# Performance work log

Measured on AMD Instinct MI355X. Metric: run time of the kernel, lower is better.

Reference implementation:

```python
import jax, jax.numpy as jnp
import numpy as np

B, N, M = 4, 2048, 2048
DIM, DIM_KEYS, DIM_OUT = 512, 512, 512
HEADS, DIM_HEAD = 8, 64
INNER = HEADS * DIM_HEAD


def setup_inputs() -> dict:
    key = jax.random.key(0)
    ks = jax.random.split(key, 8)
    x = jax.random.normal(ks[0], (B, N, DIM), dtype=jnp.float32)
    context = jax.random.normal(ks[1], (B, M, DIM_KEYS), dtype=jnp.float32)
    Wq = jax.random.normal(ks[2], (DIM, INNER), dtype=jnp.float32) / np.sqrt(DIM)
    Wkv = jax.random.normal(ks[3], (DIM_KEYS, 2 * INNER), dtype=jnp.float32) / np.sqrt(DIM_KEYS)
    null_k = jax.random.normal(ks[4], (DIM_HEAD,), dtype=jnp.float32)
    null_v = jax.random.normal(ks[5], (DIM_HEAD,), dtype=jnp.float32)
    Wout = jax.random.normal(ks[6], (INNER, DIM_OUT), dtype=jnp.float32) / np.sqrt(INNER)
    bout = jnp.zeros((DIM_OUT,), dtype=jnp.float32)
    return {"x": x, "context": context, "Wq": Wq, "Wkv": Wkv,
            "null_k": null_k, "null_v": null_v, "Wout": Wout, "bout": bout}


def reference(x, context, Wq, Wkv, null_k, null_v, Wout, bout):
    b = x.shape[0]
    scale = DIM_HEAD ** (-0.5)
    q = x @ Wq                      # [b, n, inner]
    kv = context @ Wkv              # [b, m, 2*inner]
    k, v = jnp.split(kv, 2, axis=-1)
    # [b, h, n, d]
    q = q.reshape(b, -1, HEADS, DIM_HEAD).transpose(0, 2, 1, 3)
    k = k.reshape(b, -1, HEADS, DIM_HEAD).transpose(0, 2, 1, 3)
    v = v.reshape(b, -1, HEADS, DIM_HEAD).transpose(0, 2, 1, 3)
    # prepend null key/value token: [b, h, 1, d]
    nk = jnp.broadcast_to(null_k, (b, HEADS, 1, DIM_HEAD))
    nv = jnp.broadcast_to(null_v, (b, HEADS, 1, DIM_HEAD))
    k = jnp.concatenate((nk, k), axis=-2)  # [b, h, m+1, d]
    v = jnp.concatenate((nv, v), axis=-2)
    q = jnp.tanh(q)
    k = jnp.tanh(k)
    sim = jnp.einsum('bhid,bhjd->bhij', q, k) * scale  # [b, h, n, m+1]
    attn = jax.nn.softmax(sim, axis=-1)
    out = jnp.einsum('bhij,bhjd->bhid', attn, v)       # [b, h, n, d]
    out = out.transpose(0, 2, 1, 3).reshape(b, -1, INNER)  # [b, n, inner]
    return out @ Wout + bout
```

## Files before the change

kernel.cpp:

```cpp
#include <hip/hip_runtime.h>
#include <hip/hip_bf16.h>
#include <stdint.h>

#define B_    4
#define N_    2048
#define M_    2048
#define DIMX  512
#define INNER 512
#define H_    8
#define DH    64
#define MK    2049
#define MKP   2112

#define QSCALE  0.18033688011f
#define SM_BIAS -11.5415605f

using u16 = unsigned short;
using u32 = unsigned int;

typedef __attribute__((ext_vector_type(8))) short short8;
typedef __attribute__((ext_vector_type(4))) float f32x4;

#if defined(__has_builtin)
# if __has_builtin(__builtin_amdgcn_exp2f)
#  define EXP2(x) __builtin_amdgcn_exp2f(x)
# endif
#endif
#ifndef EXP2
# define EXP2(x) exp2f(x)
#endif

__device__ __forceinline__ u16 bfc(float f){
  __hip_bfloat16 h = __float2bfloat16(f);
  return *reinterpret_cast<u16*>(&h);
}
__device__ __forceinline__ u32 bfpk(float lo, float hi){
  return (u32)bfc(lo) | ((u32)bfc(hi) << 16);
}

__global__ __launch_bounds__(256) void convert_bf(
    const float* __restrict__ x, const float* __restrict__ ctx,
    u16* __restrict__ xb, u16* __restrict__ cb)
{
  const float* in = blockIdx.z ? ctx : x;
  u16* out        = blockIdx.z ? cb : xb;
  const int i = blockIdx.x * 256 + threadIdx.x;
  float4 a = ((const float4*)in)[i*2];
  float4 b = ((const float4*)in)[i*2+1];
  uint4 t;
  t.x = bfpk(a.x, a.y); t.y = bfpk(a.z, a.w);
  t.z = bfpk(b.x, b.y); t.w = bfpk(b.z, b.w);
  ((uint4*)out)[i] = t;
}

__global__ __launch_bounds__(256) void transpose_all(
    const float* __restrict__ Wq, const float* __restrict__ Wkv,
    const float* __restrict__ Wout,
    u16* __restrict__ Wqt, u16* __restrict__ Wkvt, u16* __restrict__ Woutt)
{
  const int z = blockIdx.z;
  const float* in = (z == 0) ? Wq : (z == 1) ? Wkv : Wout;
  u16* out        = (z == 0) ? Wqt : (z == 1) ? Wkvt : Woutt;
  const int C     = (z == 1) ? 1024 : 512;
  const int R     = 512;
  if (blockIdx.x * 64 >= C) return;

  __shared__ float tl[64][65];
  const int t = threadIdx.x;
  const int c0 = blockIdx.x * 64, r0 = blockIdx.y * 64;
  const int col = t & 63, rb = t >> 6;
  #pragma unroll
  for (int j = 0; j < 16; ++j){
    const int row = rb + j*4;
    tl[row][col] = in[(size_t)(r0 + row) * C + c0 + col];
  }
  __syncthreads();
  #pragma unroll
  for (int j = 0; j < 16; ++j){
    const int orow = rb + j*4;
    out[(size_t)(c0 + orow) * R + r0 + col] = bfc(tl[col][orow]);
  }
}

#define PROJ_COMPUTE(bi)                                                      \
  {                                                                           \
    short8 af[4], bf[4];                                                      \
    _Pragma("unroll")                                                         \
    for (int m = 0; m < 4; ++m){                                              \
      const int row = wr + m*16 + c;                                          \
      af[m] = *(const short8*)((char*)At[bi] + row*64 + ((g ^ ((row>>1)&3)) << 4)); \
    }                                                                         \
    _Pragma("unroll")                                                         \
    for (int n = 0; n < 4; ++n){                                              \
      const int row = wc + n*16 + c;                                          \
      bf[n] = *(const short8*)((char*)Bl[bi] + row*64 + ((g ^ ((row>>1)&3)) << 4)); \
    }                                                                         \
    __builtin_amdgcn_s_setprio(1);                                            \
    _Pragma("unroll")                                                         \
    for (int m = 0; m < 4; ++m)                                               \
      _Pragma("unroll")                                                       \
      for (int n = 0; n < 4; ++n)                                             \
        acc[m][n] = __builtin_amdgcn_mfma_f32_16x16x32_bf16(af[m], bf[n], acc[m][n], 0, 0, 0); \
    __builtin_amdgcn_s_setprio(0);                                            \
  }

__global__ __launch_bounds__(256, 3) void fused_proj(
    const u16* __restrict__ xb, const u16* __restrict__ cb,
    const u16* __restrict__ Wqt, const u16* __restrict__ Wkvt,
    u16* __restrict__ qb, u16* __restrict__ kb, u16* __restrict__ vb)
{
  __shared__ __align__(16) short At[2][128*32];
  __shared__ __align__(16) short Bl[2][128*32];

  const int flat = blockIdx.x;
  const int tile = (flat & 7) * 96 + (flat >> 3);
  const bool isq = tile < 256;
  const int lt   = isq ? tile : tile - 256;
  const int gx   = isq ? 4 : 8;
  const int row0 = (lt / gx) * 128, col0 = (lt % gx) * 128;
  const u16* A  = isq ? xb : cb;
  const u16* Bt = isq ? Wqt : Wkvt;

  const int tid = threadIdx.x;
  const int w = tid >> 6, lane = tid & 63;
  const int c = lane & 15, g = lane >> 4;
  const int wr = (w >> 1) * 64, wc = (w & 1) * 64;

  f32x4 acc[4][4] = {};

  const int srow = tid >> 1, sj = (tid & 1) * 2;
  const int swz0 = ((sj  ) ^ ((srow >> 1) & 3)) << 4;
  const int swz1 = ((sj+1) ^ ((srow >> 1) & 3)) << 4;

  const u16* asrc = A  + (size_t)(row0 + srow) * DIMX + sj*8;
  const u16* bsrc = Bt + (size_t)(col0 + srow) * DIMX + sj*8;

  uint4 aA0, aA1, bA0, bA1;
  uint4 aB0, aB1, bB0, bB1;

  aA0 = ((const uint4*)asrc)[0];        aA1 = ((const uint4*)asrc)[1];
  bA0 = ((const uint4*)bsrc)[0];        bA1 = ((const uint4*)bsrc)[1];
  aB0 = ((const uint4*)(asrc + 32))[0]; aB1 = ((const uint4*)(asrc + 32))[1];
  bB0 = ((const uint4*)(bsrc + 32))[0]; bB1 = ((const uint4*)(bsrc + 32))[1];
  *(uint4*)((char*)At[0] + srow*64 + swz0) = aA0;
  *(uint4*)((char*)At[0] + srow*64 + swz1) = aA1;
  *(uint4*)((char*)Bl[0] + srow*64 + swz0) = bA0;
  *(uint4*)((char*)Bl[0] + srow*64 + swz1) = bA1;

  for (int kk = 0; kk < 16; kk += 2){
    __syncthreads();
    if (kk + 2 < 16){
      const u16* an = asrc + (kk+2)*32;
      const u16* bn = bsrc + (kk+2)*32;
      aA0 = ((const uint4*)an)[0]; aA1 = ((const uint4*)an)[1];
      bA0 = ((const uint4*)bn)[0]; bA1 = ((const uint4*)bn)[1];
    }
    PROJ_COMPUTE(0);
    *(uint4*)((char*)At[1] + srow*64 + swz0) = aB0;
    *(uint4*)((char*)At[1] + srow*64 + swz1) = aB1;
    *(uint4*)((char*)Bl[1] + srow*64 + swz0) = bB0;
    *(uint4*)((char*)Bl[1] + srow*64 + swz1) = bB1;

    __syncthreads();
    if (kk + 3 < 16){
      const u16* an = asrc + (kk+3)*32;
      const u16* bn = bsrc + (kk+3)*32;
      aB0 = ((const uint4*)an)[0]; aB1 = ((const uint4*)an)[1];
      bB0 = ((const uint4*)bn)[0]; bB1 = ((const uint4*)bn)[1];
    }
    PROJ_COMPUTE(1);
    if (kk + 2 < 16){
      *(uint4*)((char*)At[0] + srow*64 + swz0) = aA0;
      *(uint4*)((char*)At[0] + srow*64 + swz1) = aA1;
      *(uint4*)((char*)Bl[0] + srow*64 + swz0) = bA0;
      *(uint4*)((char*)Bl[0] + srow*64 + swz1) = bA1;
    }
  }

  #pragma unroll
  for (int m = 0; m < 4; ++m){
    #pragma unroll
    for (int n = 0; n < 4; ++n){
      #pragma unroll
      for (int rr = 0; rr < 4; ++rr){
        const int R = row0 + wr + m*16 + g*4 + rr;
        const int col = col0 + wc + n*16 + c;
        const float v = acc[m][n][rr];
        if (isq){
          qb[(size_t)R * INNER + col] = bfc(tanhf(v) * QSCALE);
        } else {
          const int bidx = R >> 11, mm = R & 2047;
          if (col < INNER){
            const int h = col >> 6, d = col & 63;
            kb[((size_t)(bidx*H_ + h) * MKP + (mm + 1)) * DH + d] = bfc(tanhf(v));
          } else {
            const int cc = col - INNER;
            const int h = cc >> 6, d = cc & 63;
            vb[((size_t)(bidx*H_ + h) * MKP + (mm + 1)) * DH + d] = bfc(v);
          }
        }
      }
    }
  }
}

__global__ __launch_bounds__(256, 3) void mgemm_out(
    const u16* __restrict__ A, const u16* __restrict__ Bt,
    float* __restrict__ Cf, const float* __restrict__ bias)
{
  __shared__ __align__(16) short At[2][128*32];
  __shared__ __align__(16) short Bl[2][128*32];

  const int flat = blockIdx.x;
  const int tile = (flat & 7) * 32 + (flat >> 3);
  const int row0 = (tile >> 2) * 128, col0 = (tile & 3) * 128;

  const int tid = threadIdx.x;
  const int w = tid >> 6, lane = tid & 63;
  const int c = lane & 15, g = lane >> 4;
  const int wr = (w >> 1) * 64, wc = (w & 1) * 64;

  f32x4 acc[4][4] = {};

  const int srow = tid >> 1, sj = (tid & 1) * 2;
  const int swz0 = ((sj  ) ^ ((srow >> 1) & 3)) << 4;
  const int swz1 = ((sj+1) ^ ((srow >> 1) & 3)) << 4;

  const u16* asrc = A  + (size_t)(row0 + srow) * INNER + sj*8;
  const u16* bsrc = Bt + (size_t)(col0 + srow) * INNER + sj*8;

  uint4 aA0, aA1, bA0, bA1;
  uint4 aB0, aB1, bB0, bB1;

  aA0 = ((const uint4*)asrc)[0];        aA1 = ((const uint4*)asrc)[1];
  bA0 = ((const uint4*)bsrc)[0];        bA1 = ((const uint4*)bsrc)[1];
  aB0 = ((const uint4*)(asrc + 32))[0]; aB1 = ((const uint4*)(asrc + 32))[1];
  bB0 = ((const uint4*)(bsrc + 32))[0]; bB1 = ((const uint4*)(bsrc + 32))[1];
  *(uint4*)((char*)At[0] + srow*64 + swz0) = aA0;
  *(uint4*)((char*)At[0] + srow*64 + swz1) = aA1;
  *(uint4*)((char*)Bl[0] + srow*64 + swz0) = bA0;
  *(uint4*)((char*)Bl[0] + srow*64 + swz1) = bA1;

  for (int kk = 0; kk < 16; kk += 2){
    __syncthreads();
    if (kk + 2 < 16){
      const u16* an = asrc + (kk+2)*32;
      const u16* bn = bsrc + (kk+2)*32;
      aA0 = ((const uint4*)an)[0]; aA1 = ((const uint4*)an)[1];
      bA0 = ((const uint4*)bn)[0]; bA1 = ((const uint4*)bn)[1];
    }
    PROJ_COMPUTE(0);
    *(uint4*)((char*)At[1] + srow*64 + swz0) = aB0;
    *(uint4*)((char*)At[1] + srow*64 + swz1) = aB1;
    *(uint4*)((char*)Bl[1] + srow*64 + swz0) = bB0;
    *(uint4*)((char*)Bl[1] + srow*64 + swz1) = bB1;

    __syncthreads();
    if (kk + 3 < 16){
      const u16* an = asrc + (kk+3)*32;
      const u16* bn = bsrc + (kk+3)*32;
      aB0 = ((const uint4*)an)[0]; aB1 = ((const uint4*)an)[1];
      bB0 = ((const uint4*)bn)[0]; bB1 = ((const uint4*)bn)[1];
    }
    PROJ_COMPUTE(1);
    if (kk + 2 < 16){
      *(uint4*)((char*)At[0] + srow*64 + swz0) = aA0;
      *(uint4*)((char*)At[0] + srow*64 + swz1) = aA1;
      *(uint4*)((char*)Bl[0] + srow*64 + swz0) = bA0;
      *(uint4*)((char*)Bl[0] + srow*64 + swz1) = bA1;
    }
  }

  #pragma unroll
  for (int m = 0; m < 4; ++m){
    #pragma unroll
    for (int n = 0; n < 4; ++n){
      #pragma unroll
      for (int rr = 0; rr < 4; ++rr){
        const int R = row0 + wr + m*16 + g*4 + rr;
        const int col = col0 + wc + n*16 + c;
        Cf[(size_t)R * 512 + col] = acc[m][n][rr] + bias[col];
      }
    }
  }
}

__global__ __launch_bounds__(256) void vtrans(
    const u16* __restrict__ vb, u16* __restrict__ vt,
    const float* __restrict__ nk, const float* __restrict__ nv,
    u16* __restrict__ kb)
{
  __shared__ short tl[64][72];
  const int t = threadIdx.x;
  const int mt = blockIdx.x, bh = blockIdx.y;
  {
    const int mr = t >> 2, chb = (t & 3) * 2;
    const u16* src = vb + ((size_t)bh * MKP + mt*64 + mr) * DH + chb*8;
    uint4 a = ((const uint4*)src)[0];
    uint4 b = ((const uint4*)src)[1];
    *(uint4*)((char*)tl + mr*144 + chb*16)     = a;
    *(uint4*)((char*)tl + mr*144 + (chb+1)*16) = b;
  }
  __syncthreads();
  {
    const int d = t >> 2, chb = (t & 3) * 2;
    #pragma unroll
    for (int j = 0; j < 2; ++j){
      const int mbase = (chb + j) * 8;
      u16 s[8];
      #pragma unroll
      for (int e = 0; e < 8; ++e) s[e] = (u16)tl[mbase + e][d];
      if (mt == 0 && mbase == 0) s[0] = bfc(nv[d]);
      uint4 o;
      o.x = (u32)s[0] | ((u32)s[1] << 16);
      o.y = (u32)s[2] | ((u32)s[3] << 16);
      o.z = (u32)s[4] | ((u32)s[5] << 16);
      o.w = (u32)s[6] | ((u32)s[7] << 16);
      *(uint4*)(vt + ((size_t)bh * DH + d) * MKP + mt*64 + mbase) = o;
    }
    if (mt == 0 && (t & 3) == 0)
      kb[(size_t)bh * MKP * DH + d] = bfc(tanhf(nk[d]));
  }
}

__global__ __launch_bounds__(256) void attn_mfma(
    const u16* __restrict__ qb, const u16* __restrict__ kb,
    const u16* __restrict__ vt, u16* __restrict__ aob)
{
  __shared__ __align__(16) short Kl[2][64*64];
  __shared__ __align__(16) short Vl[2][64*64];
  __shared__ __align__(16) short Pl[4][16*64];

  const int tid  = threadIdx.x;
  const int w    = tid >> 6;
  const int lane = tid & 63;
  const int c    = lane & 15;
  const int g    = lane >> 4;
  const int bh   = blockIdx.y, b = bh >> 3, h = bh & 7;
  const int qbase = blockIdx.x * 64 + w * 16;
  const int xr   = (c & 7) << 4;

  short8 qf0, qf1;
  {
    const u16* qrow = qb + ((size_t)(b*N_) + qbase + c) * INNER + h * DH;
    qf0 = *(const short8*)(qrow + g*8);
    qf1 = *(const short8*)(qrow + 32 + g*8);
  }

  f32x4 o[4] = {};
  float l_c = 0.f;

  const u16* kbase = kb + (size_t)bh * MKP * DH;
  const u16* vbase = vt + (size_t)bh * DH * MKP;
  const int srow = tid >> 2, sch = (tid & 3) * 2;
  const int swz0 = ((sch  ) ^ (srow & 7)) << 4;
  const int swz1 = ((sch+1) ^ (srow & 7)) << 4;

  uint4 rk0, rk1, rv0, rv1;
  {
    const u16* ksrc = kbase + (size_t)srow * DH + sch*8;
    rk0 = ((const uint4*)ksrc)[0]; rk1 = ((const uint4*)ksrc)[1];
    const u16* vsrc = vbase + (size_t)srow * MKP + sch*8;
    rv0 = ((const uint4*)vsrc)[0]; rv1 = ((const uint4*)vsrc)[1];
  }
  *(uint4*)((char*)Kl[0] + srow*128 + swz0) = rk0;
  *(uint4*)((char*)Kl[0] + srow*128 + swz1) = rk1;
  *(uint4*)((char*)Vl[0] + srow*128 + swz0) = rv0;
  *(uint4*)((char*)Vl[0] + srow*128 + swz1) = rv1;

  int cur = 0;
  for (int kt = 0; kt < 33; ++kt){
    __syncthreads();
    if (kt < 32){
      const u16* ksrc = kbase + (size_t)((kt+1)*64 + srow) * DH + sch*8;
      rk0 = ((const uint4*)ksrc)[0]; rk1 = ((const uint4*)ksrc)[1];
      const u16* vsrc = vbase + (size_t)srow * MKP + (kt+1)*64 + sch*8;
      rv0 = ((const uint4*)vsrc)[0]; rv1 = ((const uint4*)vsrc)[1];
    }

    const char* Kc = (const char*)Kl[cur];
    const char* Vc = (const char*)Vl[cur];
    char*       Pw = (char*)Pl + w*2048;

    f32x4 sv[4];
    __builtin_amdgcn_s_setprio(1);
    #pragma unroll
    for (int s = 0; s < 4; ++s){
      f32x4 a = {SM_BIAS, SM_BIAS, SM_BIAS, SM_BIAS};
      #pragma unroll
      for (int hh = 0; hh < 2; ++hh){
        short8 kf = *(const short8*)(Kc + (s*16 + c)*128 + ((hh*64 + g*16) ^ xr));
        a = __builtin_amdgcn_mfma_f32_16x16x32_bf16(kf, hh ? qf1 : qf0, a, 0, 0, 0);
      }
      sv[s] = a;
    }
    __builtin_amdgcn_s_setprio(0);

    if (kt == 32){
      #pragma unroll
      for (int s = 0; s < 4; ++s)
        #pragma unroll
        for (int r = 0; r < 4; ++r)
          if (s | r) sv[s][r] = -1e30f;
      if (g) sv[0][0] = -1e30f;
    }

    float psum = 0.f;
    #pragma unroll
    for (int s = 0; s < 4; ++s){
      const float p0 = EXP2(sv[s][0]);
      const float p1 = EXP2(sv[s][1]);
      const float p2 = EXP2(sv[s][2]);
      const float p3 = EXP2(sv[s][3]);
      psum += (p0 + p1) + (p2 + p3);
      uint2 pk;
      pk.x = bfpk(p0, p1);
      pk.y = bfpk(p2, p3);
      *(uint2*)(Pw + c*128 + ((((2*s + (g>>1)) ^ (c&7)) << 4) | ((g&1)*8))) = pk;
    }
    psum += __shfl_xor(psum, 16);
    psum += __shfl_xor(psum, 32);
    l_c += psum;

    __builtin_amdgcn_s_setprio(1);
    #pragma unroll
    for (int hh = 0; hh < 2; ++hh){
      short8 pf = *(const short8*)(Pw + c*128 + (((hh*4 + g) ^ (c&7)) << 4));
      #pragma unroll
      for (int D = 0; D < 4; ++D){
        short8 vf = *(const short8*)(Vc + (D*16 + c)*128 + ((hh*64 + g*16) ^ xr));
        o[D] = __builtin_amdgcn_mfma_f32_16x16x32_bf16(pf, vf, o[D], 0, 0, 0);
      }
    }
    __builtin_amdgcn_s_setprio(0);

    if (kt < 32){
      char* Kn = (char*)Kl[cur ^ 1];
      char* Vn = (char*)Vl[cur ^ 1];
      *(uint4*)(Kn + srow*128 + swz0) = rk0;
      *(uint4*)(Kn + srow*128 + swz1) = rk1;
      *(uint4*)(Vn + srow*128 + swz0) = rv0;
      *(uint4*)(Vn + srow*128 + swz1) = rv1;
      cur ^= 1;
    }
  }

  const float inv = 1.f / l_c;
  #pragma unroll
  for (int r = 0; r < 4; ++r){
    const float ir = __shfl(inv, g*4 + r, 16);
    const size_t nrow = (size_t)(b*N_) + qbase + g*4 + r;
    #pragma unroll
    for (int D = 0; D < 4; ++D)
      aob[nrow * INNER + h*DH + D*16 + c] = bfc(o[D][r] * ir);
  }
}

extern "C" void kernel_launch(void* const* d_in, const int* in_sizes, int n_in,
                              void* d_out, int out_size, void* d_ws, size_t ws_size,
                              hipStream_t stream)
{
  const float* x    = (const float*)d_in[0];
  const float* ctx  = (const float*)d_in[1];
  const float* Wq   = (const float*)d_in[2];
  const float* Wkv  = (const float*)d_in[3];
  const float* nk   = (const float*)d_in[4];
  const float* nv   = (const float*)d_in[5];
  const float* Wout = (const float*)d_in[6];
  const float* bout = (const float*)d_in[7];
  float* out = (float*)d_out;

  char* ws = (char*)d_ws;
  u16* xb    = (u16*)(ws);
  u16* cb    = (u16*)(ws +  8388608);
  u16* qb    = (u16*)(ws + 16777216);
  u16* kbB   = (u16*)(ws + 25165824);
  u16* vbB   = (u16*)(ws + 33816576);
  u16* vtb   = (u16*)(ws + 42467328);
  u16* Wqt   = (u16*)(ws + 51118080);
  u16* Wkvt  = (u16*)(ws + 51642368);
  u16* Woutt = (u16*)(ws + 52690944);
  u16* aoB   = vbB;

  convert_bf<<<dim3(2048, 1, 2), 256, 0, stream>>>(x, ctx, xb, cb);
  transpose_all<<<dim3(16, 8, 3), 256, 0, stream>>>(Wq, Wkv, Wout, Wqt, Wkvt, Woutt);

  fused_proj<<<768, 256, 0, stream>>>(xb, cb, Wqt, Wkvt, qb, kbB, vbB);
  vtrans<<<dim3(33, 32), 256, 0, stream>>>(vbB, vtb, nk, nv, kbB);
  attn_mfma<<<dim3(32, 32), 256, 0, stream>>>(qb, kbB, vtb, aoB);
  mgemm_out<<<256, 256, 0, stream>>>(aoB, Woutt, out, bout);
}
```

Measured before the change: 118.5 us.

## Fuse fp32-to-bf16 conversion into projection GEMM; process two query tiles per attention wave

Removes the standalone convert_bf kernel so the projection GEMM loads fp32 x/context directly and packs them to bf16 before storing to LDS. This avoids writing and re-reading the intermediate bf16 copies, but doubles the global A-operand bytes read inside the GEMM and adds register pressure. Separately, each attention wave now handles 32 query rows instead of 16, so every K/V tile loaded into LDS feeds twice as many MFMAs, halving the grid. The cost is more registers and half as many blocks, which may hurt occupancy.

```diff
diff --git a/kernel.cpp b/kernel.cpp
--- a/kernel.cpp
+++ b/kernel.cpp
@@ -36,21 +36,6 @@
 }
 __device__ __forceinline__ u32 bfpk(float lo, float hi){
   return (u32)bfc(lo) | ((u32)bfc(hi) << 16);
-}
-
-__global__ __launch_bounds__(256) void convert_bf(
-    const float* __restrict__ x, const float* __restrict__ ctx,
-    u16* __restrict__ xb, u16* __restrict__ cb)
-{
-  const float* in = blockIdx.z ? ctx : x;
-  u16* out        = blockIdx.z ? cb : xb;
-  const int i = blockIdx.x * 256 + threadIdx.x;
-  float4 a = ((const float4*)in)[i*2];
-  float4 b = ((const float4*)in)[i*2+1];
-  uint4 t;
-  t.x = bfpk(a.x, a.y); t.y = bfpk(a.z, a.w);
-  t.z = bfpk(b.x, b.y); t.w = bfpk(b.z, b.w);
-  ((uint4*)out)[i] = t;
 }
 
 __global__ __launch_bounds__(256) void transpose_all(
@@ -104,8 +89,14 @@
     __builtin_amdgcn_s_setprio(0);                                            \
   }
 
+#define PACK_A(t0, t1, q0, q1, q2, q3)                                        \
+  t0.x = bfpk(q0.x, q0.y); t0.y = bfpk(q0.z, q0.w);                           \
+  t0.z = bfpk(q1.x, q1.y); t0.w = bfpk(q1.z, q1.w);                           \
+  t1.x = bfpk(q2.x, q2.y); t1.y = bfpk(q2.z, q2.w);                           \
+  t1.z = bfpk(q3.x, q3.y); t1.w = bfpk(q3.z, q3.w);
+
 __global__ __launch_bounds__(256, 3) void fused_proj(
-    const u16* __restrict__ xb, const u16* __restrict__ cb,
+    const float* __restrict__ x, const float* __restrict__ ctx,
     const u16* __restrict__ Wqt, const u16* __restrict__ Wkvt,
     u16* __restrict__ qb, u16* __restrict__ kb, u16* __restrict__ vb)
 {
@@ -118,8 +109,8 @@
   const int lt   = isq ? tile : tile - 256;
   const int gx   = isq ? 4 : 8;
   const int row0 = (lt / gx) * 128, col0 = (lt % gx) * 128;
-  const u16* A  = isq ? xb : cb;
-  const u16* Bt = isq ? Wqt : Wkvt;
+  const float* A = isq ? x : ctx;
+  const u16*  Bt = isq ? Wqt : Wkvt;
 
   const int tid = threadIdx.x;
   const int w = tid >> 6, lane = tid & 63;
@@ -132,46 +123,63 @@
   const int swz0 = ((sj  ) ^ ((srow >> 1) & 3)) << 4;
   const int swz1 = ((sj+1) ^ ((srow >> 1) & 3)) << 4;
 
-  const u16* asrc = A  + (size_t)(row0 + srow) * DIMX + sj*8;
-  const u16* bsrc = Bt + (size_t)(col0 + srow) * DIMX + sj*8;
-
-  uint4 aA0, aA1, bA0, bA1;
-  uint4 aB0, aB1, bB0, bB1;
-
-  aA0 = ((const uint4*)asrc)[0];        aA1 = ((const uint4*)asrc)[1];
-  bA0 = ((const uint4*)bsrc)[0];        bA1 = ((const uint4*)bsrc)[1];
-  aB0 = ((const uint4*)(asrc + 32))[0]; aB1 = ((const uint4*)(asrc + 32))[1];
-  bB0 = ((const uint4*)(bsrc + 32))[0]; bB1 = ((const uint4*)(bsrc + 32))[1];
-  *(uint4*)((char*)At[0] + srow*64 + swz0) = aA0;
-  *(uint4*)((char*)At[0] + srow*64 + swz1) = aA1;
-  *(uint4*)((char*)Bl[0] + srow*64 + swz0) = bA0;
-  *(uint4*)((char*)Bl[0] + srow*64 + swz1) = bA1;
+  const float* asrc = A  + (size_t)(row0 + srow) * DIMX + sj*8;
+  const u16*   bsrc = Bt + (size_t)(col0 + srow) * DIMX + sj*8;
+
+  float4 aA0, aA1, aA2, aA3;  uint4 bA0, bA1;
+  float4 aB0, aB1, aB2, aB3;  uint4 bB0, bB1;
+
+  aA0 = ((const float4*)asrc)[0]; aA1 = ((const float4*)asrc)[1];
+  aA2 = ((const float4*)asrc)[2]; aA3 = ((const float4*)asrc)[3];
+  bA0 = ((const uint4*)bsrc)[0];  bA1 = ((const uint4*)bsrc)[1];
+  {
+    const float* an = asrc + 32;
+    aB0 = ((const float4*)an)[0]; aB1 = ((const float4*)an)[1];
+    aB2 = ((const float4*)an)[2]; aB3 = ((const float4*)an)[3];
+    bB0 = ((const uint4*)(bsrc + 32))[0]; bB1 = ((const uint4*)(bsrc + 32))[1];
+  }
+  {
+    uint4 t0, t1;
+    PACK_A(t0, t1, aA0, aA1, aA2, aA3);
+    *(uint4*)((char*)At[0] + srow*64 + swz0) = t0;
+    *(uint4*)((char*)At[0] + srow*64 + swz1) = t1;
+    *(uint4*)((char*)Bl[0] + srow*64 + swz0) = bA0;
+    *(uint4*)((char*)Bl[0] + srow*64 + swz1) = bA1;
+  }
 
   for (int kk = 0; kk < 16; kk += 2){
     __syncthreads();
     if (kk + 2 < 16){
-      const u16* an = asrc + (kk+2)*32;
-      const u16* bn = bsrc + (kk+2)*32;
-      aA0 = ((const uint4*)an)[0]; aA1 = ((const uint4*)an)[1];
-      bA0 = ((const uint4*)bn)[0]; bA1 = ((const uint4*)bn)[1];
+      const float* an = asrc + (kk+2)*32;
+      const u16*   bn = bsrc + (kk+2)*32;
+      aA0 = ((const float4*)an)[0]; aA1 = ((const float4*)an)[1];
+      aA2 = ((const float4*)an)[2]; aA3 = ((const float4*)an)[3];
+      bA0 = ((const uint4*)bn)[0];  bA1 = ((const uint4*)bn)[1];
     }
     PROJ_COMPUTE(0);
-    *(uint4*)((char*)At[1] + srow*64 + swz0) = aB0;
-    *(uint4*)((char*)At[1] + srow*64 + swz1) = aB1;
-    *(uint4*)((char*)Bl[1] + srow*64 + swz0) = bB0;
-    *(uint4*)((char*)Bl[1] + srow*64 + swz1) = bB1;
+    {
+      uint4 t0, t1;
+      PACK_A(t0, t1, aB0, aB1, aB2, aB3);
+      *(uint4*)((char*)At[1] + srow*64 + swz0) = t0;
+      *(uint4*)((char*)At[1] + srow*64 + swz1) = t1;
+      *(uint4*)((char*)Bl[1] + srow*64 + swz0) = bB0;
+      *(uint4*)((char*)Bl[1] + srow*64 + swz1) = bB1;
+    }
 
     __syncthreads();
     if (kk + 3 < 16){
-      const u16* an = asrc + (kk+3)*32;
-      const u16* bn = bsrc + (kk+3)*32;
-      aB0 = ((const uint4*)an)[0]; aB1 = ((const uint4*)an)[1];
-      bB0 = ((const uint4*)bn)[0]; bB1 = ((const uint4*)bn)[1];
+      const float* an = asrc + (kk+3)*32;
+      const u16*   bn = bsrc + (kk+3)*32;
+      aB0 = ((const float4*)an)[0]; aB1 = ((const float4*)an)[1];
+      aB2 = ((const float4*)an)[2]; aB3 = ((const float4*)an)[3];
+      bB0 = ((const uint4*)bn)[0];  bB1 = ((const uint4*)bn)[1];
     }
     PROJ_COMPUTE(1);
     if (kk + 2 < 16){
-      *(uint4*)((char*)At[0] + srow*64 + swz0) = aA0;
-      *(uint4*)((char*)At[0] + srow*64 + swz1) = aA1;
+      uint4 t0, t1;
+      PACK_A(t0, t1, aA0, aA1, aA2, aA3);
+      *(uint4*)((char*)At[0] + srow*64 + swz0) = t0;
+      *(uint4*)((char*)At[0] + srow*64 + swz1) = t1;
       *(uint4*)((char*)Bl[0] + srow*64 + swz0) = bA0;
       *(uint4*)((char*)Bl[0] + srow*64 + swz1) = bA1;
     }
@@ -329,7 +337,7 @@
 {
   __shared__ __align__(16) short Kl[2][64*64];
   __shared__ __align__(16) short Vl[2][64*64];
-  __shared__ __align__(16) short Pl[4][16*64];
+  __shared__ __align__(16) short Pl[4][32*64];
 
   const int tid  = threadIdx.x;
   const int w    = tid >> 6;
@@ -337,18 +345,19 @@
   const int c    = lane & 15;
   const int g    = lane >> 4;
   const int bh   = blockIdx.y, b = bh >> 3, h = bh & 7;
-  const int qbase = blockIdx.x * 64 + w * 16;
+  const int qbase = blockIdx.x * 128 + w * 32;
   const int xr   = (c & 7) << 4;
 
-  short8 qf0, qf1;
-  {
-    const u16* qrow = qb + ((size_t)(b*N_) + qbase + c) * INNER + h * DH;
-    qf0 = *(const short8*)(qrow + g*8);
-    qf1 = *(const short8*)(qrow + 32 + g*8);
-  }
-
-  f32x4 o[4] = {};
-  float l_c = 0.f;
+  short8 qf[2][2];
+  #pragma unroll
+  for (int u = 0; u < 2; ++u){
+    const u16* qrow = qb + ((size_t)(b*N_) + qbase + u*16 + c) * INNER + h * DH;
+    qf[u][0] = *(const short8*)(qrow + g*8);
+    qf[u][1] = *(const short8*)(qrow + 32 + g*8);
+  }
+
+  f32x4 o[2][4] = {};
+  float l0 = 0.f, l1 = 0.f;
 
   const u16* kbase = kb + (size_t)bh * MKP * DH;
   const u16* vbase = vt + (size_t)bh * DH * MKP;
@@ -380,56 +389,67 @@
 
     const char* Kc = (const char*)Kl[cur];
     const char* Vc = (const char*)Vl[cur];
-    char*       Pw = (char*)Pl + w*2048;
-
-    f32x4 sv[4];
+    char*       Pw = (char*)Pl + w*4096;
+
+    f32x4 sv[2][4];
     __builtin_amdgcn_s_setprio(1);
     #pragma unroll
     for (int s = 0; s < 4; ++s){
-      f32x4 a = {SM_BIAS, SM_BIAS, SM_BIAS, SM_BIAS};
-      #pragma unroll
-      for (int hh = 0; hh < 2; ++hh){
-        short8 kf = *(const short8*)(Kc + (s*16 + c)*128 + ((hh*64 + g*16) ^ xr));
-        a = __builtin_amdgcn_mfma_f32_16x16x32_bf16(kf, hh ? qf1 : qf0, a, 0, 0, 0);
+      const int row = s*16 + c;
+      short8 kf0 = *(const short8*)(Kc + row*128 + ((     g*16) ^ xr));
+      short8 kf1 = *(const short8*)(Kc + row*128 + ((64 + g*16) ^ xr));
+      f32x4 a0 = {SM_BIAS, SM_BIAS, SM_BIAS, SM_BIAS};
+      f32x4 a1 = {SM_BIAS, SM_BIAS, SM_BIAS, SM_BIAS};
+      a0 = __builtin_amdgcn_mfma_f32_16x16x32_bf16(kf0, qf[0][0], a0, 0, 0, 0);
+      a1 = __builtin_amdgcn_mfma_f32_16x16x32_bf16(kf0, qf[1][0], a1, 0, 0, 0);
+      a0 = __builtin_amdgcn_mfma_f32_16x16x32_bf16(kf1, qf[0][1], a0, 0, 0, 0);
+      a1 = __builtin_amdgcn_mfma_f32_16x16x32_bf16(kf1, qf[1][1], a1, 0, 0, 0);
+      sv[0][s] = a0; sv[1][s] = a1;
+    }
+    __builtin_amdgcn_s_setprio(0);
+
+    if (kt == 32){
+      #pragma unroll
+      for (int u = 0; u < 2; ++u)
+        #pragma unroll
+        for (int s = 0; s < 4; ++s)
+          #pragma unroll
+          for (int r = 0; r < 4; ++r)
+            if (s | r) sv[u][s][r] = -1e30f;
+      if (g){ sv[0][0][0] = -1e30f; sv[1][0][0] = -1e30f; }
+    }
+
+    #pragma unroll
+    for (int u = 0; u < 2; ++u){
+      float psum = 0.f;
+      #pragma unroll
+      for (int s = 0; s < 4; ++s){
+        const float p0 = EXP2(sv[u][s][0]);
+        const float p1 = EXP2(sv[u][s][1]);
+        const float p2 = EXP2(sv[u][s][2]);
+        const float p3 = EXP2(sv[u][s][3]);
+        psum += (p0 + p1) + (p2 + p3);
+        uint2 pk;
+        pk.x = bfpk(p0, p1);
+        pk.y = bfpk(p2, p3);
+        *(uint2*)(Pw + (u*16 + c)*128
+                  + ((((2*s + (g>>1)) ^ (c&7)) << 4) | ((g&1)*8))) = pk;
       }
-      sv[s] = a;
-    }
-    __builtin_amdgcn_s_setprio(0);
-
-    if (kt == 32){
-      #pragma unroll
-      for (int s = 0; s < 4; ++s)
-        #pragma unroll
-        for (int r = 0; r < 4; ++r)
-          if (s | r) sv[s][r] = -1e30f;
-      if (g) sv[0][0] = -1e30f;
-    }
-
-    float psum = 0.f;
-    #pragma unroll
-    for (int s = 0; s < 4; ++s){
-      const float p0 = EXP2(sv[s][0]);
-      const float p1 = EXP2(sv[s][1]);
-      const float p2 = EXP2(sv[s][2]);
-      const float p3 = EXP2(sv[s][3]);
-      psum += (p0 + p1) + (p2 + p3);
-      uint2 pk;
-      pk.x = bfpk(p0, p1);
-      pk.y = bfpk(p2, p3);
-      *(uint2*)(Pw + c*128 + ((((2*s + (g>>1)) ^ (c&7)) << 4) | ((g&1)*8))) = pk;
-    }
-    psum += __shfl_xor(psum, 16);
-    psum += __shfl_xor(psum, 32);
-    l_c += psum;
+      psum += __shfl_xor(psum, 16);
+      psum += __shfl_xor(psum, 32);
+      if (u == 0) l0 += psum; else l1 += psum;
+    }
 
     __builtin_amdgcn_s_setprio(1);
     #pragma unroll
     for (int hh = 0; hh < 2; ++hh){
-      short8 pf = *(const short8*)(Pw + c*128 + (((hh*4 + g) ^ (c&7)) << 4));
+      short8 pf0 = *(const short8*)(Pw + (     c)*128 + (((hh*4 + g) ^ (c&7)) << 4));
+      short8 pf1 = *(const short8*)(Pw + (16 + c)*128 + (((hh*4 + g) ^ (c&7)) << 4));
       #pragma unroll
       for (int D = 0; D < 4; ++D){
         short8 vf = *(const short8*)(Vc + (D*16 + c)*128 + ((hh*64 + g*16) ^ xr));
-        o[D] = __builtin_amdgcn_mfma_f32_16x16x32_bf16(pf, vf, o[D], 0, 0, 0);
+        o[0][D] = __builtin_amdgcn_mfma_f32_16x16x32_bf16(pf0, vf, o[0][D], 0, 0, 0);
+        o[1][D] = __builtin_amdgcn_mfma_f32_16x16x32_bf16(pf1, vf, o[1][D], 0, 0, 0);
       }
     }
     __builtin_amdgcn_s_setprio(0);
@@ -445,14 +465,17 @@
     }
   }
 
-  const float inv = 1.f / l_c;
   #pragma unroll
-  for (int r = 0; r < 4; ++r){
-    const float ir = __shfl(inv, g*4 + r, 16);
-    const size_t nrow = (size_t)(b*N_) + qbase + g*4 + r;
-    #pragma unroll
-    for (int D = 0; D < 4; ++D)
-      aob[nrow * INNER + h*DH + D*16 + c] = bfc(o[D][r] * ir);
+  for (int u = 0; u < 2; ++u){
+    const float inv = 1.f / (u ? l1 : l0);
+    #pragma unroll
+    for (int r = 0; r < 4; ++r){
+      const float ir = __shfl(inv, g*4 + r, 16);
+      const size_t nrow = (size_t)(b*N_) + qbase + u*16 + g*4 + r;
+      #pragma unroll
+      for (int D = 0; D < 4; ++D)
+        aob[nrow * INNER + h*DH + D*16 + c] = bfc(o[u][D][r] * ir);
+    }
   }
 }
 
@@ -471,22 +494,19 @@
   float* out = (float*)d_out;
 
   char* ws = (char*)d_ws;
-  u16* xb    = (u16*)(ws);
-  u16* cb    = (u16*)(ws +  8388608);
-  u16* qb    = (u16*)(ws + 16777216);
-  u16* kbB   = (u16*)(ws + 25165824);
-  u16* vbB   = (u16*)(ws + 33816576);
-  u16* vtb   = (u16*)(ws + 42467328);
-  u16* Wqt   = (u16*)(ws + 51118080);
-  u16* Wkvt  = (u16*)(ws + 51642368);
-  u16* Woutt = (u16*)(ws + 52690944);
+  u16* qb    = (u16*)(ws);
+  u16* kbB   = (u16*)(ws +  8388608);
+  u16* vbB   = (u16*)(ws + 17039360);
+  u16* vtb   = (u16*)(ws + 25690112);
+  u16* Wqt   = (u16*)(ws + 34340864);
+  u16* Wkvt  = (u16*)(ws + 34865152);
+  u16* Woutt = (u16*)(ws + 35913728);
   u16* aoB   = vbB;
 
-  convert_bf<<<dim3(2048, 1, 2), 256, 0, stream>>>(x, ctx, xb, cb);
   transpose_all<<<dim3(16, 8, 3), 256, 0, stream>>>(Wq, Wkv, Wout, Wqt, Wkvt, Woutt);
 
-  fused_proj<<<768, 256, 0, stream>>>(xb, cb, Wqt, Wkvt, qb, kbB, vbB);
+  fused_proj<<<768, 256, 0, stream>>>(x, ctx, Wqt, Wkvt, qb, kbB, vbB);
   vtrans<<<dim3(33, 32), 256, 0, stream>>>(vbB, vtb, nk, nv, kbB);
-  attn_mfma<<<dim3(32, 32), 256, 0, stream>>>(qb, kbB, vtb, aoB);
+  attn_mfma<<<dim3(16, 32), 256, 0, stream>>>(qb, kbB, vtb, aoB);
   mgemm_out<<<256, 256, 0, stream>>>(aoB, Woutt, out, bout);
 }
```

Measured after the change: 117.0 us. About the same (-1.3%).

## Process two 16-row query tiles per wave to reuse K/V fragments

Applied to the files above, without the earlier changes.

Each wave in the attention kernel now handles 32 query rows instead of 16, so each block covers 128 queries and the grid is halved. K and V fragments read from shared memory are reused across two MFMA accumulators, which cuts LDS reads and global K/V tile loads per query. The cost is higher register pressure, a doubled P buffer in shared memory, and only 512 blocks, which may lower occupancy and leave the 256 CUs less evenly loaded.

```diff
diff --git a/kernel.cpp b/kernel.cpp
--- a/kernel.cpp
+++ b/kernel.cpp
@@ -329,7 +329,7 @@
 {
   __shared__ __align__(16) short Kl[2][64*64];
   __shared__ __align__(16) short Vl[2][64*64];
-  __shared__ __align__(16) short Pl[4][16*64];
+  __shared__ __align__(16) short Pl[4][32*64];
 
   const int tid  = threadIdx.x;
   const int w    = tid >> 6;
@@ -337,18 +337,19 @@
   const int c    = lane & 15;
   const int g    = lane >> 4;
   const int bh   = blockIdx.y, b = bh >> 3, h = bh & 7;
-  const int qbase = blockIdx.x * 64 + w * 16;
+  const int qbase = blockIdx.x * 128 + w * 32;
   const int xr   = (c & 7) << 4;
 
-  short8 qf0, qf1;
-  {
-    const u16* qrow = qb + ((size_t)(b*N_) + qbase + c) * INNER + h * DH;
-    qf0 = *(const short8*)(qrow + g*8);
-    qf1 = *(const short8*)(qrow + 32 + g*8);
-  }
-
-  f32x4 o[4] = {};
-  float l_c = 0.f;
+  short8 qf[2][2];
+  #pragma unroll
+  for (int u = 0; u < 2; ++u){
+    const u16* qrow = qb + ((size_t)(b*N_) + qbase + u*16 + c) * INNER + h * DH;
+    qf[u][0] = *(const short8*)(qrow + g*8);
+    qf[u][1] = *(const short8*)(qrow + 32 + g*8);
+  }
+
+  f32x4 o[2][4] = {};
+  float l0 = 0.f, l1 = 0.f;
 
   const u16* kbase = kb + (size_t)bh * MKP * DH;
   const u16* vbase = vt + (size_t)bh * DH * MKP;
@@ -380,56 +381,67 @@
 
     const char* Kc = (const char*)Kl[cur];
     const char* Vc = (const char*)Vl[cur];
-    char*       Pw = (char*)Pl + w*2048;
-
-    f32x4 sv[4];
+    char*       Pw = (char*)Pl + w*4096;
+
+    f32x4 sv[2][4];
     __builtin_amdgcn_s_setprio(1);
     #pragma unroll
     for (int s = 0; s < 4; ++s){
-      f32x4 a = {SM_BIAS, SM_BIAS, SM_BIAS, SM_BIAS};
-      #pragma unroll
-      for (int hh = 0; hh < 2; ++hh){
-        short8 kf = *(const short8*)(Kc + (s*16 + c)*128 + ((hh*64 + g*16) ^ xr));
-        a = __builtin_amdgcn_mfma_f32_16x16x32_bf16(kf, hh ? qf1 : qf0, a, 0, 0, 0);
+      const int row = s*16 + c;
+      short8 kf0 = *(const short8*)(Kc + row*128 + ((     g*16) ^ xr));
+      short8 kf1 = *(const short8*)(Kc + row*128 + ((64 + g*16) ^ xr));
+      f32x4 a0 = {SM_BIAS, SM_BIAS, SM_BIAS, SM_BIAS};
+      f32x4 a1 = {SM_BIAS, SM_BIAS, SM_BIAS, SM_BIAS};
+      a0 = __builtin_amdgcn_mfma_f32_16x16x32_bf16(kf0, qf[0][0], a0, 0, 0, 0);
+      a1 = __builtin_amdgcn_mfma_f32_16x16x32_bf16(kf0, qf[1][0], a1, 0, 0, 0);
+      a0 = __builtin_amdgcn_mfma_f32_16x16x32_bf16(kf1, qf[0][1], a0, 0, 0, 0);
+      a1 = __builtin_amdgcn_mfma_f32_16x16x32_bf16(kf1, qf[1][1], a1, 0, 0, 0);
+      sv[0][s] = a0; sv[1][s] = a1;
+    }
+    __builtin_amdgcn_s_setprio(0);
+
+    if (kt == 32){
+      #pragma unroll
+      for (int u = 0; u < 2; ++u)
+        #pragma unroll
+        for (int s = 0; s < 4; ++s)
+          #pragma unroll
+          for (int r = 0; r < 4; ++r)
+            if (s | r) sv[u][s][r] = -1e30f;
+      if (g){ sv[0][0][0] = -1e30f; sv[1][0][0] = -1e30f; }
+    }
+
+    #pragma unroll
+    for (int u = 0; u < 2; ++u){
+      float psum = 0.f;
+      #pragma unroll
+      for (int s = 0; s < 4; ++s){
+        const float p0 = EXP2(sv[u][s][0]);
+        const float p1 = EXP2(sv[u][s][1]);
+        const float p2 = EXP2(sv[u][s][2]);
+        const float p3 = EXP2(sv[u][s][3]);
+        psum += (p0 + p1) + (p2 + p3);
+        uint2 pk;
+        pk.x = bfpk(p0, p1);
+        pk.y = bfpk(p2, p3);
+        *(uint2*)(Pw + (u*16 + c)*128
+                  + ((((2*s + (g>>1)) ^ (c&7)) << 4) | ((g&1)*8))) = pk;
       }
-      sv[s] = a;
-    }
-    __builtin_amdgcn_s_setprio(0);
-
-    if (kt == 32){
-      #pragma unroll
-      for (int s = 0; s < 4; ++s)
-        #pragma unroll
-        for (int r = 0; r < 4; ++r)
-          if (s | r) sv[s][r] = -1e30f;
-      if (g) sv[0][0] = -1e30f;
-    }
-
-    float psum = 0.f;
-    #pragma unroll
-    for (int s = 0; s < 4; ++s){
-      const float p0 = EXP2(sv[s][0]);
-      const float p1 = EXP2(sv[s][1]);
-      const float p2 = EXP2(sv[s][2]);
-      const float p3 = EXP2(sv[s][3]);
-      psum += (p0 + p1) + (p2 + p3);
-      uint2 pk;
-      pk.x = bfpk(p0, p1);
-      pk.y = bfpk(p2, p3);
-      *(uint2*)(Pw + c*128 + ((((2*s + (g>>1)) ^ (c&7)) << 4) | ((g&1)*8))) = pk;
-    }
-    psum += __shfl_xor(psum, 16);
-    psum += __shfl_xor(psum, 32);
-    l_c += psum;
+      psum += __shfl_xor(psum, 16);
+      psum += __shfl_xor(psum, 32);
+      if (u == 0) l0 += psum; else l1 += psum;
+    }
 
     __builtin_amdgcn_s_setprio(1);
     #pragma unroll
     for (int hh = 0; hh < 2; ++hh){
-      short8 pf = *(const short8*)(Pw + c*128 + (((hh*4 + g) ^ (c&7)) << 4));
+      short8 pf0 = *(const short8*)(Pw + (     c)*128 + (((hh*4 + g) ^ (c&7)) << 4));
+      short8 pf1 = *(const short8*)(Pw + (16 + c)*128 + (((hh*4 + g) ^ (c&7)) << 4));
       #pragma unroll
       for (int D = 0; D < 4; ++D){
         short8 vf = *(const short8*)(Vc + (D*16 + c)*128 + ((hh*64 + g*16) ^ xr));
-        o[D] = __builtin_amdgcn_mfma_f32_16x16x32_bf16(pf, vf, o[D], 0, 0, 0);
+        o[0][D] = __builtin_amdgcn_mfma_f32_16x16x32_bf16(pf0, vf, o[0][D], 0, 0, 0);
+        o[1][D] = __builtin_amdgcn_mfma_f32_16x16x32_bf16(pf1, vf, o[1][D], 0, 0, 0);
       }
     }
     __builtin_amdgcn_s_setprio(0);
@@ -445,14 +457,17 @@
     }
   }
 
-  const float inv = 1.f / l_c;
   #pragma unroll
-  for (int r = 0; r < 4; ++r){
-    const float ir = __shfl(inv, g*4 + r, 16);
-    const size_t nrow = (size_t)(b*N_) + qbase + g*4 + r;
-    #pragma unroll
-    for (int D = 0; D < 4; ++D)
-      aob[nrow * INNER + h*DH + D*16 + c] = bfc(o[D][r] * ir);
+  for (int u = 0; u < 2; ++u){
+    const float inv = 1.f / (u ? l1 : l0);
+    #pragma unroll
+    for (int r = 0; r < 4; ++r){
+      const float ir = __shfl(inv, g*4 + r, 16);
+      const size_t nrow = (size_t)(b*N_) + qbase + u*16 + g*4 + r;
+      #pragma unroll
+      for (int D = 0; D < 4; ++D)
+        aob[nrow * INNER + h*DH + D*16 + c] = bfc(o[u][D][r] * ir);
+    }
   }
 }
 
@@ -487,6 +502,6 @@
 
   fused_proj<<<768, 256, 0, stream>>>(xb, cb, Wqt, Wkvt, qb, kbB, vbB);
   vtrans<<<dim3(33, 32), 256, 0, stream>>>(vbB, vtb, nk, nv, kbB);
-  attn_mfma<<<dim3(32, 32), 256, 0, stream>>>(qb, kbB, vtb, aoB);
+  attn_mfma<<<dim3(16, 32), 256, 0, stream>>>(qb, kbB, vtb, aoB);
   mgemm_out<<<256, 256, 0, stream>>>(aoB, Woutt, out, bout);
 }
```

New measurement: 113.9 us. 1.04x faster.
